# Optimization experiments

Measured on AMD Instinct MI355X. Metric: run time of the kernel, lower is better.

Reference implementation:

```python
import jax, jax.numpy as jnp
import numpy as np

IN_C, HID_C, OUT_C = 256, 512, 256
B, N = 8, 4096


def setup_inputs() -> dict:
    key = jax.random.key(0)
    ks = jax.random.split(key, 6)
    x = jax.random.normal(ks[0], (B, N, IN_C), dtype=jnp.float32)
    A = jax.random.uniform(ks[1], (B, N, N), dtype=jnp.float32)
    # Glorot-ish init for the two GCN layer weights + zero biases (PyG default bias=True)
    W1 = jax.random.normal(ks[2], (IN_C, HID_C), dtype=jnp.float32) * (1.0 / np.sqrt(IN_C))
    b1 = jnp.zeros((HID_C,), dtype=jnp.float32)
    W2 = jax.random.normal(ks[3], (HID_C, OUT_C), dtype=jnp.float32) * (1.0 / np.sqrt(HID_C))
    b2 = jnp.zeros((OUT_C,), dtype=jnp.float32)
    return {"x": x, "A": A, "W1": W1, "b1": b1, "W2": W2, "b2": b2}


def _gcn_norm(A):
    # dense equivalent of PyG gcn_norm with add_self_loops: A_hat = A + I,
    # norm = D^{-1/2} A_hat D^{-1/2}, with deg==0 -> 0 (inf guarded)
    A_hat = A + jnp.eye(A.shape[-1], dtype=A.dtype)  # [B,N,N]
    deg = A_hat.sum(axis=-1)                          # [B,N]
    d_inv_sqrt = jnp.where(deg > 0, jax.lax.rsqrt(jnp.maximum(deg, 1e-12)), 0.0)
    return d_inv_sqrt[:, :, None] * A_hat * d_inv_sqrt[:, None, :]


def reference(x, A, W1, b1, W2, b2):
    nrm = _gcn_norm(A)  # [B,N,N]
    # layer 1: out = A_hat_norm @ (x W1) + b1, then ReLU (dropout is identity in eval)
    h = jax.nn.relu(jnp.einsum('bij,bjh->bih', nrm, x @ W1) + b1)
    # layer 2
    out = jnp.einsum('bij,bjo->bio', nrm, h @ W2) + b2
    return out
```

## Files before the change

kernel.cpp:

```cpp
#include <hip/hip_runtime.h>
#include <stdint.h>

#define NN   4096
#define BATCH 8
#define IC   256
#define HC   512
#define OC   256

typedef float    f32x4  __attribute__((ext_vector_type(4)));
typedef __bf16   bf16x8 __attribute__((ext_vector_type(8)));
typedef uint16_t u16x8  __attribute__((ext_vector_type(8)));
typedef uint16_t u16x4  __attribute__((ext_vector_type(4)));

__device__ __forceinline__ uint16_t f2b(float f) {
  union { float f; uint32_t u; } v; v.f = f;
  return (uint16_t)((v.u + 0x7FFFu + ((v.u >> 16) & 1u)) >> 16);
}

__device__ __forceinline__ void gl_lds16(const void* g, void* l) {
  __builtin_amdgcn_global_load_lds(
      (const __attribute__((address_space(1))) uint32_t*)g,
      (__attribute__((address_space(3))) uint32_t*)l, 16, 0, 0);
}

__global__ __launch_bounds__(256) void deg_kernel(const float* __restrict__ A,
                                                  float* __restrict__ dinv) {
  const int row = blockIdx.x;
  const float* ap = A + (size_t)row * NN;
  const int t = threadIdx.x;
  float s = 0.f;
#pragma unroll
  for (int i = 0; i < 4; ++i) {
    f32x4 v = *(const f32x4*)(ap + (t + 256 * i) * 4);
    s += v[0] + v[1] + v[2] + v[3];
  }
#pragma unroll
  for (int off = 32; off > 0; off >>= 1) s += __shfl_xor(s, off, 64);
  __shared__ float red[4];
  if ((t & 63) == 0) red[t >> 6] = s;
  __syncthreads();
  if (t == 0) {
    float deg = red[0] + red[1] + red[2] + red[3] + 1.0f;
    dinv[row] = 1.0f / sqrtf(deg);
  }
}

__global__ __launch_bounds__(256) void prep_kernel(const float* __restrict__ A,
                                                   const float* __restrict__ dinv,
                                                   uint16_t* __restrict__ Anorm) {
  const int bid = blockIdx.x;
  const int b = bid & 7, mt = (bid >> 3) & 63, kq = bid >> 9;
  const int t = threadIdx.x;
  const float* Ab = A + ((size_t)b * NN + mt * 64) * NN;
  const float* dv = dinv + b * NN;
  uint16_t* out = Anorm + ((size_t)(b * 64 + mt)) * 64 * 4096;
  for (int kt = kq * 16; kt < kq * 16 + 16; ++kt) {
#pragma unroll
    for (int it = 0; it < 2; ++it) {
      int tt = it * 256 + t;
      int r = tt >> 3, g = tt & 7;
      int i = mt * 64 + r;
      int j0 = kt * 64 + g * 8;
      const float* ap = Ab + (size_t)r * NN + j0;
      f32x4 a0 = *(const f32x4*)ap;
      f32x4 a1 = *(const f32x4*)(ap + 4);
      float dvi = dv[i];
      f32x4 d0 = *(const f32x4*)(dv + j0);
      f32x4 d1 = *(const f32x4*)(dv + j0 + 4);
      int dj = i - j0;
      u16x8 o;
#pragma unroll
      for (int e = 0; e < 4; ++e) {
        float v0 = (a0[e] + ((dj == e) ? 1.f : 0.f)) * dvi * d0[e];
        float v1 = (a1[e] + ((dj == e + 4) ? 1.f : 0.f)) * dvi * d1[e];
        o[e] = f2b(v0);
        o[e + 4] = f2b(v1);
      }
      *(u16x8*)(out + ((size_t)kt * 64 + r) * 64 + (g ^ (r & 7)) * 8) = o;
    }
  }
}

template<bool ABF16, int KTOT, int NC>
__global__ __launch_bounds__(256, 2) void xw_kernel(const void* __restrict__ Av,
                                                    const float* __restrict__ W,
                                                    uint16_t* __restrict__ Vt) {
  constexpr int LDT = 72;
  __shared__ uint16_t smem[18432];
  uint16_t* as_ = smem;
  uint16_t* wt_ = smem + 9216;
  const int t = threadIdx.x;
  const int m0 = blockIdx.x * 128;
  const int n0 = blockIdx.y * 128;
  const int lane = t & 63, wid = t >> 6;
  const int wm = wid >> 1, wn = wid & 1;
  f32x4 acc[4][4] = {};

  for (int kt = 0; kt < KTOT / 64; ++kt) {
    const int k0 = kt * 64;
    __syncthreads();
    if constexpr (!ABF16) {
      const float* Ap = (const float*)Av;
      const int c4 = t & 15, r0 = t >> 4;
#pragma unroll
      for (int i = 0; i < 8; ++i) {
        int r = r0 + 16 * i;
        f32x4 v = *(const f32x4*)(Ap + (size_t)(m0 + r) * KTOT + k0 + c4 * 4);
        uint32_t lo = f2b(v[0]) | ((uint32_t)f2b(v[1]) << 16);
        uint32_t hi = f2b(v[2]) | ((uint32_t)f2b(v[3]) << 16);
        *(uint2*)&as_[r * LDT + c4 * 4] = make_uint2(lo, hi);
      }
    } else {
      const uint16_t* Ap = (const uint16_t*)Av;
      const int c8 = t & 7, r0 = t >> 3;
#pragma unroll
      for (int i = 0; i < 4; ++i) {
        int r = r0 + 32 * i;
        u16x8 v = *(const u16x8*)(Ap + (size_t)(m0 + r) * KTOT + k0 + c8 * 8);
        *(u16x8*)&as_[r * LDT + c8 * 8] = v;
      }
    }
    {
      const int n4 = t & 31, kq = t >> 5;
#pragma unroll
      for (int i = 0; i < 8; ++i) {
        int k = kq + 8 * i;
        f32x4 v = *(const f32x4*)(W + (size_t)(k0 + k) * NC + n0 + n4 * 4);
        uint16_t hv[4] = { f2b(v[0]), f2b(v[1]), f2b(v[2]), f2b(v[3]) };
#pragma unroll
        for (int w = 0; w < 4; ++w) {
          int we = (w + n4) & 3;
          wt_[(n4 * 4 + we) * LDT + k] = hv[we];
        }
      }
    }
    __syncthreads();
#pragma unroll
    for (int kk = 0; kk < 2; ++kk) {
      bf16x8 bfr[4], afr[4];
#pragma unroll
      for (int fn = 0; fn < 4; ++fn)
        bfr[fn] = *(const bf16x8*)&wt_[(wn * 64 + fn * 16 + (lane & 15)) * LDT + kk * 32 + (lane >> 4) * 8];
#pragma unroll
      for (int fm = 0; fm < 4; ++fm)
        afr[fm] = *(const bf16x8*)&as_[(wm * 64 + fm * 16 + (lane & 15)) * LDT + kk * 32 + (lane >> 4) * 8];
#pragma unroll
      for (int fm = 0; fm < 4; ++fm)
#pragma unroll
        for (int fn = 0; fn < 4; ++fn)
          acc[fm][fn] = __builtin_amdgcn_mfma_f32_16x16x32_bf16(afr[fm], bfr[fn], acc[fm][fn], 0, 0, 0);
    }
  }
  const int b = m0 >> 12;
  const int kl0 = m0 & 4095;
  __syncthreads();
  uint16_t* lv = smem;
#pragma unroll
  for (int fm = 0; fm < 4; ++fm)
#pragma unroll
    for (int fn = 0; fn < 4; ++fn) {
      int nloc = wn * 64 + fn * 16 + (lane & 15);
      int ml0  = wm * 64 + fm * 16 + (lane >> 4) * 4;
      u16x4 pk;
      pk[0] = f2b(acc[fm][fn][0]); pk[1] = f2b(acc[fm][fn][1]);
      pk[2] = f2b(acc[fm][fn][2]); pk[3] = f2b(acc[fm][fn][3]);
      *(u16x4*)&lv[nloc * 144 + ml0] = pk;
    }
  __syncthreads();
#pragma unroll
  for (int i = 0; i < 8; ++i) {
    int nloc = (t >> 4) + 16 * i;
    int ch = t & 15;
    u16x8 v = *(const u16x8*)&lv[nloc * 144 + ch * 8];
    int nglob = n0 + nloc;
    int ktv = (kl0 >> 6) + (ch >> 3);
    int s = (ch & 7) ^ (nglob & 7);
    *(u16x8*)(Vt + (((size_t)b * 64 + ktv) * NC + nglob) * 64 + s * 8) = v;
  }
}

template<int BN_, bool RELU>
__global__ __launch_bounds__(BN_, 4) void agg_kernel(const uint16_t* __restrict__ Anorm,
                                                     const uint16_t* __restrict__ Vt,
                                                     const float* __restrict__ bias,
                                                     uint16_t* __restrict__ Hout,
                                                     float* __restrict__ Fout) {
  constexpr int NWAVES = BN_ / 64;
  __shared__ uint16_t as_[64 * 64];
  __shared__ uint16_t vt_[BN_ * 64];
  const int t = threadIdx.x;
  const int lane = t & 63, wid = t >> 6;
  const int bid = blockIdx.x;
  const int b = bid & 7, mt = bid >> 3;
  const int fr = lane & 15, c = lane >> 4;

  const uint16_t* Abase = Anorm + ((size_t)(b * 64 + mt)) * 64 * 4096;
  const uint16_t* Vbase = Vt + (size_t)b * 64 * BN_ * 64;

  f32x4 acc[4][4] = {};

  for (int kt = 0; kt < 64; ++kt) {
    __syncthreads();
    const uint16_t* At    = Abase + (size_t)kt * 4096;
    const uint16_t* Vtile = Vbase + (size_t)kt * (BN_ * 64);
    for (int ca = wid; ca < 8; ca += NWAVES)
      gl_lds16(At + ca * 512 + lane * 8, &as_[ca * 512]);
#pragma unroll
    for (int i = 0; i < 8; ++i) {
      int cv = wid * 8 + i;
      gl_lds16(Vtile + cv * 512 + lane * 8, &vt_[cv * 512]);
    }
    __syncthreads();
#pragma unroll
    for (int kk = 0; kk < 2; ++kk) {
      bf16x8 afr[4], bfr[4];
#pragma unroll
      for (int fm = 0; fm < 4; ++fm) {
        int row = fm * 16 + fr;
        afr[fm] = *(const bf16x8*)&as_[row * 64 + (((kk << 2) + c) ^ (row & 7)) * 8];
      }
#pragma unroll
      for (int fn = 0; fn < 4; ++fn) {
        int n = wid * 64 + fn * 16 + fr;
        bfr[fn] = *(const bf16x8*)&vt_[n * 64 + (((kk << 2) + c) ^ (n & 7)) * 8];
      }
#pragma unroll
      for (int fm = 0; fm < 4; ++fm)
#pragma unroll
        for (int fn = 0; fn < 4; ++fn)
          acc[fm][fn] = __builtin_amdgcn_mfma_f32_16x16x32_bf16(afr[fm], bfr[fn], acc[fm][fn], 0, 0, 0);
    }
  }
#pragma unroll
  for (int fm = 0; fm < 4; ++fm)
#pragma unroll
    for (int r = 0; r < 4; ++r) {
      size_t grow = (size_t)b * NN + mt * 64 + fm * 16 + (lane >> 4) * 4 + r;
#pragma unroll
      for (int fn = 0; fn < 4; ++fn) {
        int col = wid * 64 + fn * 16 + fr;
        float v = acc[fm][fn][r] + bias[col];
        if constexpr (RELU) {
          Hout[grow * BN_ + col] = f2b(fmaxf(v, 0.f));
        } else {
          Fout[grow * BN_ + col] = v;
        }
      }
    }
}

extern "C" void kernel_launch(void* const* d_in, const int* in_sizes, int n_in,
                              void* d_out, int out_size, void* d_ws, size_t ws_size,
                              hipStream_t stream) {
  const float* x  = (const float*)d_in[0];
  const float* A  = (const float*)d_in[1];
  const float* W1 = (const float*)d_in[2];
  const float* b1 = (const float*)d_in[3];
  const float* W2 = (const float*)d_in[4];
  const float* b2 = (const float*)d_in[5];
  float* out = (float*)d_out;

  char* ws = (char*)d_ws;
  uint16_t* Anorm = (uint16_t*)ws;
  float*    dinv  = (float*)(ws + 268435456);
  uint16_t* Vt    = (uint16_t*)(ws + 268435456 + 131072);
  uint16_t* H     = (uint16_t*)(ws + 268435456 + 131072 + 33554432);

  deg_kernel<<<BATCH * NN, 256, 0, stream>>>(A, dinv);
  prep_kernel<<<2048, 256, 0, stream>>>(A, dinv, Anorm);
  xw_kernel<false, IC, HC><<<dim3(256, 4), 256, 0, stream>>>(x, W1, Vt);
  agg_kernel<HC, true><<<512, 512, 0, stream>>>(Anorm, Vt, b1, H, nullptr);
  xw_kernel<true, HC, OC><<<dim3(256, 2), 256, 0, stream>>>(H, W2, Vt);
  agg_kernel<OC, false><<<512, 256, 0, stream>>>(Anorm, Vt, b2, nullptr, out);
}
```

Measured before the change: 1.203 ms.

## Fuse degree and bf16 conversion, fold D^-1/2 scaling into GEMM epilogues, double-buffer aggregation

Merges the degree reduction into the A-to-bf16 conversion pass, so A (the dominant 512MB input) is read once instead of twice. The D^-1/2 normalization moves out of the stored matrix: column scaling goes into the XW epilogue and row scaling into the aggregation epilogue. The aggregation kernel gains 128-row tiles, 8 waves, a K-step of 32, LDS double buffering with async global-to-LDS loads, and s_setprio around the MFMAs to overlap loads with compute. In exchange there are more barriers per K step, the Vt layout changes, and the prep kernel launches only 256 large blocks, which may underutilize the device.

```diff
diff --git a/kernel.cpp b/kernel.cpp
--- a/kernel.cpp
+++ b/kernel.cpp
@@ -1,11 +1,12 @@
 #include <hip/hip_runtime.h>
 #include <stdint.h>
 
-#define NN   4096
+#define NN    4096
 #define BATCH 8
-#define IC   256
-#define HC   512
-#define OC   256
+#define IC    256
+#define HC    512
+#define OC    256
+#define MTOT  (BATCH * NN)
 
 typedef float    f32x4  __attribute__((ext_vector_type(4)));
 typedef __bf16   bf16x8 __attribute__((ext_vector_type(8)));
@@ -23,67 +24,45 @@
       (__attribute__((address_space(3))) uint32_t*)l, 16, 0, 0);
 }
 
-__global__ __launch_bounds__(256) void deg_kernel(const float* __restrict__ A,
-                                                  float* __restrict__ dinv) {
-  const int row = blockIdx.x;
-  const float* ap = A + (size_t)row * NN;
+__global__ __launch_bounds__(512) void prep_kernel(const float* __restrict__ A,
+                                                   uint16_t* __restrict__ Abf,
+                                                   float* __restrict__ dinv) {
+  const int bid = blockIdx.x;
+  const int b = bid & 7, mt = bid >> 3;
   const int t = threadIdx.x;
+  const int r = t >> 2, g = t & 3;
+  const int rowl = mt * 128 + r;
+  const float* Ap = A + ((size_t)b * NN + rowl) * NN + g * 8;
+  uint16_t* Op = Abf + ((size_t)(b * 32 + mt) << 19) + r * 32 + ((g ^ (r & 3)) << 3);
   float s = 0.f;
-#pragma unroll
-  for (int i = 0; i < 4; ++i) {
-    f32x4 v = *(const f32x4*)(ap + (t + 256 * i) * 4);
-    s += v[0] + v[1] + v[2] + v[3];
-  }
-#pragma unroll
-  for (int off = 32; off > 0; off >>= 1) s += __shfl_xor(s, off, 64);
-  __shared__ float red[4];
-  if ((t & 63) == 0) red[t >> 6] = s;
+  for (int kt = 0; kt < 128; ++kt) {
+    f32x4 a0 = *(const f32x4*)(Ap + kt * 32);
+    f32x4 a1 = *(const f32x4*)(Ap + kt * 32 + 4);
+    int dj = rowl - (kt * 32 + g * 8);
+    u16x8 o;
+#pragma unroll
+    for (int e = 0; e < 4; ++e) {
+      float v0 = a0[e], v1 = a1[e];
+      s += v0 + v1;
+      if (dj == e)     v0 += 1.f;
+      if (dj == e + 4) v1 += 1.f;
+      o[e] = f2b(v0); o[e + 4] = f2b(v1);
+    }
+    *(u16x8*)(Op + (size_t)kt * 4096) = o;
+  }
+  __shared__ float red[512];
+  red[t] = s;
   __syncthreads();
-  if (t == 0) {
-    float deg = red[0] + red[1] + red[2] + red[3] + 1.0f;
-    dinv[row] = 1.0f / sqrtf(deg);
-  }
-}
-
-__global__ __launch_bounds__(256) void prep_kernel(const float* __restrict__ A,
-                                                   const float* __restrict__ dinv,
-                                                   uint16_t* __restrict__ Anorm) {
-  const int bid = blockIdx.x;
-  const int b = bid & 7, mt = (bid >> 3) & 63, kq = bid >> 9;
-  const int t = threadIdx.x;
-  const float* Ab = A + ((size_t)b * NN + mt * 64) * NN;
-  const float* dv = dinv + b * NN;
-  uint16_t* out = Anorm + ((size_t)(b * 64 + mt)) * 64 * 4096;
-  for (int kt = kq * 16; kt < kq * 16 + 16; ++kt) {
-#pragma unroll
-    for (int it = 0; it < 2; ++it) {
-      int tt = it * 256 + t;
-      int r = tt >> 3, g = tt & 7;
-      int i = mt * 64 + r;
-      int j0 = kt * 64 + g * 8;
-      const float* ap = Ab + (size_t)r * NN + j0;
-      f32x4 a0 = *(const f32x4*)ap;
-      f32x4 a1 = *(const f32x4*)(ap + 4);
-      float dvi = dv[i];
-      f32x4 d0 = *(const f32x4*)(dv + j0);
-      f32x4 d1 = *(const f32x4*)(dv + j0 + 4);
-      int dj = i - j0;
-      u16x8 o;
-#pragma unroll
-      for (int e = 0; e < 4; ++e) {
-        float v0 = (a0[e] + ((dj == e) ? 1.f : 0.f)) * dvi * d0[e];
-        float v1 = (a1[e] + ((dj == e + 4) ? 1.f : 0.f)) * dvi * d1[e];
-        o[e] = f2b(v0);
-        o[e + 4] = f2b(v1);
-      }
-      *(u16x8*)(out + ((size_t)kt * 64 + r) * 64 + (g ^ (r & 7)) * 8) = o;
-    }
+  if (t < 128) {
+    float deg = red[t * 4] + red[t * 4 + 1] + red[t * 4 + 2] + red[t * 4 + 3] + 1.0f;
+    dinv[b * NN + mt * 128 + t] = 1.0f / sqrtf(deg);
   }
 }
 
 template<bool ABF16, int KTOT, int NC>
 __global__ __launch_bounds__(256, 2) void xw_kernel(const void* __restrict__ Av,
                                                     const float* __restrict__ W,
+                                                    const float* __restrict__ dinv,
                                                     uint16_t* __restrict__ Vt) {
   constexpr int LDT = 72;
   __shared__ uint16_t smem[18432];
@@ -152,7 +131,7 @@
     }
   }
   const int b = m0 >> 12;
-  const int kl0 = m0 & 4095;
+  const int klocal = m0 & 4095;
   __syncthreads();
   uint16_t* lv = smem;
 #pragma unroll
@@ -162,8 +141,9 @@
       int nloc = wn * 64 + fn * 16 + (lane & 15);
       int ml0  = wm * 64 + fm * 16 + (lane >> 4) * 4;
       u16x4 pk;
-      pk[0] = f2b(acc[fm][fn][0]); pk[1] = f2b(acc[fm][fn][1]);
-      pk[2] = f2b(acc[fm][fn][2]); pk[3] = f2b(acc[fm][fn][3]);
+#pragma unroll
+      for (int r = 0; r < 4; ++r)
+        pk[r] = f2b(acc[fm][fn][r] * dinv[m0 + ml0 + r]);
       *(u16x4*)&lv[nloc * 144 + ml0] = pk;
     }
   __syncthreads();
@@ -173,77 +153,96 @@
     int ch = t & 15;
     u16x8 v = *(const u16x8*)&lv[nloc * 144 + ch * 8];
     int nglob = n0 + nloc;
-    int ktv = (kl0 >> 6) + (ch >> 3);
-    int s = (ch & 7) ^ (nglob & 7);
-    *(u16x8*)(Vt + (((size_t)b * 64 + ktv) * NC + nglob) * 64 + s * 8) = v;
-  }
-}
-
-template<int BN_, bool RELU>
-__global__ __launch_bounds__(BN_, 4) void agg_kernel(const uint16_t* __restrict__ Anorm,
+    int ktv = (klocal >> 5) + (ch >> 2);
+    int s = (ch & 3) ^ (nglob & 3);
+    *(u16x8*)(Vt + (((size_t)b * 128 + ktv) * NC + nglob) * 32 + s * 8) = v;
+  }
+}
+
+template<int NC_, bool RELU>
+__global__ __launch_bounds__(512, 2) void agg_kernel(const uint16_t* __restrict__ Abf,
                                                      const uint16_t* __restrict__ Vt,
+                                                     const float* __restrict__ dinv,
                                                      const float* __restrict__ bias,
                                                      uint16_t* __restrict__ Hout,
                                                      float* __restrict__ Fout) {
-  constexpr int NWAVES = BN_ / 64;
-  __shared__ uint16_t as_[64 * 64];
-  __shared__ uint16_t vt_[BN_ * 64];
+  constexpr int FN  = NC_ / 64;
+  constexpr int WNE = NC_ / 4;
+  constexpr int VPW = NC_ / 128;
+  __shared__ uint16_t as_[2][4096];
+  __shared__ uint16_t vt_[2][NC_ * 32];
+
   const int t = threadIdx.x;
   const int lane = t & 63, wid = t >> 6;
+  const int wm = wid >> 2, wn = wid & 3;
+  const int fr = lane & 15, c = lane >> 4;
   const int bid = blockIdx.x;
   const int b = bid & 7, mt = bid >> 3;
-  const int fr = lane & 15, c = lane >> 4;
-
-  const uint16_t* Abase = Anorm + ((size_t)(b * 64 + mt)) * 64 * 4096;
-  const uint16_t* Vbase = Vt + (size_t)b * 64 * BN_ * 64;
-
-  f32x4 acc[4][4] = {};
-
-  for (int kt = 0; kt < 64; ++kt) {
-    __syncthreads();
-    const uint16_t* At    = Abase + (size_t)kt * 4096;
-    const uint16_t* Vtile = Vbase + (size_t)kt * (BN_ * 64);
-    for (int ca = wid; ca < 8; ca += NWAVES)
-      gl_lds16(At + ca * 512 + lane * 8, &as_[ca * 512]);
-#pragma unroll
-    for (int i = 0; i < 8; ++i) {
-      int cv = wid * 8 + i;
-      gl_lds16(Vtile + cv * 512 + lane * 8, &vt_[cv * 512]);
-    }
-    __syncthreads();
-#pragma unroll
-    for (int kk = 0; kk < 2; ++kk) {
-      bf16x8 afr[4], bfr[4];
-#pragma unroll
-      for (int fm = 0; fm < 4; ++fm) {
-        int row = fm * 16 + fr;
-        afr[fm] = *(const bf16x8*)&as_[row * 64 + (((kk << 2) + c) ^ (row & 7)) * 8];
-      }
-#pragma unroll
-      for (int fn = 0; fn < 4; ++fn) {
-        int n = wid * 64 + fn * 16 + fr;
-        bfr[fn] = *(const bf16x8*)&vt_[n * 64 + (((kk << 2) + c) ^ (n & 7)) * 8];
-      }
-#pragma unroll
-      for (int fm = 0; fm < 4; ++fm)
-#pragma unroll
-        for (int fn = 0; fn < 4; ++fn)
-          acc[fm][fn] = __builtin_amdgcn_mfma_f32_16x16x32_bf16(afr[fm], bfr[fn], acc[fm][fn], 0, 0, 0);
+
+  const uint16_t* Abase = Abf + ((size_t)(b * 32 + mt) << 19);
+  const uint16_t* Vbase = Vt + (size_t)b * NC_ * 4096;
+
+  auto stage = [&](int kt, int buf) {
+    const uint16_t* At = Abase + (size_t)kt * 4096;
+    const uint16_t* Vtile = Vbase + (size_t)kt * (NC_ * 32);
+    gl_lds16(At + wid * 512 + lane * 8, &as_[buf][wid * 512]);
+#pragma unroll
+    for (int i = 0; i < VPW; ++i) {
+      int cv = wid * VPW + i;
+      gl_lds16(Vtile + cv * 512 + lane * 8, &vt_[buf][cv * 512]);
+    }
+  };
+
+  f32x4 acc[4][FN] = {};
+
+  stage(0, 0);
+  asm volatile("s_waitcnt vmcnt(0)" ::: "memory");
+  asm volatile("" ::: "memory");
+  __builtin_amdgcn_s_barrier();
+  __builtin_amdgcn_sched_barrier(0);
+
+  for (int kt = 0; kt < 128; ++kt) {
+    const int cur = kt & 1;
+    if (kt < 127) stage(kt + 1, cur ^ 1);
+    bf16x8 afr[4], bfr[FN];
+#pragma unroll
+    for (int fm = 0; fm < 4; ++fm) {
+      int row = wm * 64 + fm * 16 + fr;
+      afr[fm] = *(const bf16x8*)&as_[cur][row * 32 + ((c ^ (row & 3)) << 3)];
+    }
+#pragma unroll
+    for (int fn = 0; fn < FN; ++fn) {
+      int n = wn * WNE + fn * 16 + fr;
+      bfr[fn] = *(const bf16x8*)&vt_[cur][n * 32 + ((c ^ (n & 3)) << 3)];
+    }
+    __builtin_amdgcn_s_setprio(1);
+#pragma unroll
+    for (int fm = 0; fm < 4; ++fm)
+#pragma unroll
+      for (int fn = 0; fn < FN; ++fn)
+        acc[fm][fn] = __builtin_amdgcn_mfma_f32_16x16x32_bf16(afr[fm], bfr[fn], acc[fm][fn], 0, 0, 0);
+    __builtin_amdgcn_s_setprio(0);
+    if (kt < 127) {
+      asm volatile("s_waitcnt vmcnt(0)" ::: "memory");
+      asm volatile("" ::: "memory");
+      __builtin_amdgcn_s_barrier();
+      __builtin_amdgcn_sched_barrier(0);
     }
   }
 #pragma unroll
   for (int fm = 0; fm < 4; ++fm)
 #pragma unroll
     for (int r = 0; r < 4; ++r) {
-      size_t grow = (size_t)b * NN + mt * 64 + fm * 16 + (lane >> 4) * 4 + r;
-#pragma unroll
-      for (int fn = 0; fn < 4; ++fn) {
-        int col = wid * 64 + fn * 16 + fr;
-        float v = acc[fm][fn][r] + bias[col];
+      size_t grow = (size_t)b * NN + mt * 128 + wm * 64 + fm * 16 + (lane >> 4) * 4 + r;
+      float dv = dinv[grow];
+#pragma unroll
+      for (int fn = 0; fn < FN; ++fn) {
+        int col = wn * WNE + fn * 16 + fr;
+        float v = acc[fm][fn][r] * dv + bias[col];
         if constexpr (RELU) {
-          Hout[grow * BN_ + col] = f2b(fmaxf(v, 0.f));
+          Hout[grow * NC_ + col] = f2b(fmaxf(v, 0.f));
         } else {
-          Fout[grow * BN_ + col] = v;
+          Fout[grow * NC_ + col] = v;
         }
       }
     }
@@ -261,15 +260,14 @@
   float* out = (float*)d_out;
 
   char* ws = (char*)d_ws;
-  uint16_t* Anorm = (uint16_t*)ws;
-  float*    dinv  = (float*)(ws + 268435456);
-  uint16_t* Vt    = (uint16_t*)(ws + 268435456 + 131072);
-  uint16_t* H     = (uint16_t*)(ws + 268435456 + 131072 + 33554432);
-
-  deg_kernel<<<BATCH * NN, 256, 0, stream>>>(A, dinv);
-  prep_kernel<<<2048, 256, 0, stream>>>(A, dinv, Anorm);
-  xw_kernel<false, IC, HC><<<dim3(256, 4), 256, 0, stream>>>(x, W1, Vt);
-  agg_kernel<HC, true><<<512, 512, 0, stream>>>(Anorm, Vt, b1, H, nullptr);
-  xw_kernel<true, HC, OC><<<dim3(256, 2), 256, 0, stream>>>(H, W2, Vt);
-  agg_kernel<OC, false><<<512, 256, 0, stream>>>(Anorm, Vt, b2, nullptr, out);
-}
+  uint16_t* Abf  = (uint16_t*)ws;
+  float*    dinv = (float*)(ws + 268435456);
+  uint16_t* Vt   = (uint16_t*)(ws + 268435456 + 131072);
+  uint16_t* H    = (uint16_t*)(ws + 268435456 + 131072 + 33554432);
+
+  prep_kernel<<<256, 512, 0, stream>>>(A, Abf, dinv);
+  xw_kernel<false, IC, HC><<<dim3(256, 4), 256, 0, stream>>>(x, W1, dinv, Vt);
+  agg_kernel<HC, true><<<256, 512, 0, stream>>>(Abf, Vt, dinv, b1, H, nullptr);
+  xw_kernel<true, HC, OC><<<dim3(256, 2), 256, 0, stream>>>(H, W2, dinv, Vt);
+  agg_kernel<OC, false><<<256, 512, 0, stream>>>(Abf, Vt, dinv, b2, nullptr, out);
+}
```

Result: slower. 1.234 ms (+2.6%).
